# Kernel optimization log

Hardware: AMD Instinct MI355X
Metric: run time of the kernel (lower is better)

## Reference

```python
import jax, jax.numpy as jnp
import numpy as np

B, L, T, H, NH, NQ = 4096, 64, 48, 64, 4, 3
HD = H // NH  # head dim = 16


def lstm_layer(x, h0, c0, Wih, Whh, bih, bhh):
    # x: (B, S, I); h0, c0: (B, H). PyTorch gate order: i, f, g, o.
    def step(carry, xt):
        h, c = carry
        g = xt @ Wih.T + bih + h @ Whh.T + bhh
        i, f, gg, o = jnp.split(g, 4, axis=-1)
        c = jax.nn.sigmoid(f) * c + jax.nn.sigmoid(i) * jnp.tanh(gg)
        h = jax.nn.sigmoid(o) * jnp.tanh(c)
        return (h, c), h
    (hT, cT), hs = jax.lax.scan(step, (h0, c0), jnp.swapaxes(x, 0, 1))
    return jnp.swapaxes(hs, 0, 1), hT, cT


def lstm2(x, params, h0, c0):
    # params: list of 2 tuples (Wih, Whh, bih, bhh); h0, c0: (2, B, H)
    out = x
    hs, cs = [], []
    for l in range(2):
        Wih, Whh, bih, bhh = params[l]
        out, h, c = lstm_layer(out, h0[l], c0[l], Wih, Whh, bih, bhh)
        hs.append(h)
        cs.append(c)
    return out, jnp.stack(hs), jnp.stack(cs)


def mha(q, k, v, Wqkv, bqkv, Wo, bo):
    # PyTorch nn.MultiheadAttention, batch_first, averaged attn weights.
    Wq, Wk, Wv = jnp.split(Wqkv, 3, axis=0)
    bq, bk, bv = jnp.split(bqkv, 3, axis=0)
    def heads(t):
        b, s, _ = t.shape
        return t.reshape(b, s, NH, HD)
    qh = heads(q @ Wq.T + bq)
    kh = heads(k @ Wk.T + bk)
    vh = heads(v @ Wv.T + bv)
    scores = jnp.einsum('bqhd,bkhd->bhqk', qh, kh) / jnp.sqrt(jnp.float32(HD))
    w = jax.nn.softmax(scores, axis=-1)                      # (B, NH, Sq, Sk)
    out = jnp.einsum('bhqk,bkhd->bqhd', w, vh).reshape(q.shape[0], q.shape[1], H)
    return out @ Wo.T + bo, w.mean(axis=1)                   # averaged over heads


def setup_inputs() -> dict:
    key = jax.random.key(0)
    ks = iter(jax.random.split(key, 32))
    s = 0.08
    d = {
        'x': jax.random.normal(next(ks), (B, L, H), jnp.float32),
        'target': jax.random.normal(next(ks), (B, T, H), jnp.float32),
    }
    for pre in ('enc', 'dec'):
        for l in range(2):
            d[f'{pre}_Wih{l}'] = jax.random.normal(next(ks), (4 * H, H), jnp.float32) * s
            d[f'{pre}_Whh{l}'] = jax.random.normal(next(ks), (4 * H, H), jnp.float32) * s
            d[f'{pre}_bih{l}'] = jnp.zeros((4 * H,), jnp.float32)
            d[f'{pre}_bhh{l}'] = jnp.zeros((4 * H,), jnp.float32)
    d['attn_Wqkv'] = jax.random.normal(next(ks), (3 * H, H), jnp.float32) * s
    d['attn_bqkv'] = jnp.zeros((3 * H,), jnp.float32)
    d['attn_Wo'] = jax.random.normal(next(ks), (H, H), jnp.float32) * s
    d['attn_bo'] = jnp.zeros((H,), jnp.float32)
    d['fc_W1'] = jax.random.normal(next(ks), (H // 2, H), jnp.float32) * s
    d['fc_b1'] = jnp.zeros((H // 2,), jnp.float32)
    d['fc_W2'] = jax.random.normal(next(ks), (NQ, H // 2), jnp.float32) * s
    d['fc_b2'] = jnp.zeros((NQ,), jnp.float32)
    return d


def reference(x, target,
              enc_Wih0, enc_Whh0, enc_bih0, enc_bhh0,
              enc_Wih1, enc_Whh1, enc_bih1, enc_bhh1,
              dec_Wih0, dec_Whh0, dec_bih0, dec_bhh0,
              dec_Wih1, dec_Whh1, dec_bih1, dec_bhh1,
              attn_Wqkv, attn_bqkv, attn_Wo, attn_bo,
              fc_W1, fc_b1, fc_W2, fc_b2):
    enc_p = [(enc_Wih0, enc_Whh0, enc_bih0, enc_bhh0),
             (enc_Wih1, enc_Whh1, enc_bih1, enc_bhh1)]
    dec_p = [(dec_Wih0, dec_Whh0, dec_bih0, dec_bhh0),
             (dec_Wih1, dec_Whh1, dec_bih1, dec_bhh1)]
    z = jnp.zeros((2, x.shape[0], H), x.dtype)
    enc_out, h_n, c_n = lstm2(x, enc_p, z, z)               # (B, L, H)
    attn0, _ = mha(enc_out, enc_out, enc_out, attn_Wqkv, attn_bqkv, attn_Wo, attn_bo)
    # teacher forcing: step t>=1 consumes target[:, t-1]; step 0 the attended encoder summary
    dec_in = jnp.concatenate([attn0[:, -1:, :], target[:, :-1, :]], axis=1)  # (B, T, H)
    dec_out, _, _ = lstm2(dec_in, dec_p, h_n, c_n)          # (B, T, H)
    attn_out, attn_w = mha(dec_out, enc_out, enc_out, attn_Wqkv, attn_bqkv, attn_Wo, attn_bo)
    pred = jax.nn.relu(attn_out @ fc_W1.T + fc_b1) @ fc_W2.T + fc_b2  # (B, T, 3)
    return pred, attn_w                                      # (B,T,3), (B,T,L)
```

## Files before the change

kernel.cpp:

```cpp
#include <hip/hip_runtime.h>
#include <hip/hip_bf16.h>
#include <cstddef>


#define B_   4096
#define L_   64
#define T_   48
#define H_   64
#define ROWS 16
#define PADH 136

using half8  = __attribute__((ext_vector_type(8))) _Float16;
using half4  = __attribute__((ext_vector_type(4))) _Float16;
using f32x4  = __attribute__((ext_vector_type(4))) float;

#define IC_ 4.8828125e-4f

__device__ __forceinline__ float fsig(float x) {
    return __builtin_amdgcn_rcpf(1.0f + __expf(-x));
}
__device__ __forceinline__ float ftanh(float x) {
    float e = __expf(-2.0f * fabsf(x));
    float r = (1.0f - e) * __builtin_amdgcn_rcpf(1.0f + e);
    return copysignf(r, x);
}

__global__ void transpose_w_all_kernel(
    const float* __restrict__ W0i, const float* __restrict__ W0h,
    const float* __restrict__ W1i, const float* __restrict__ W1h,
    const float* __restrict__ W2i, const float* __restrict__ W2h,
    const float* __restrict__ W3i, const float* __restrict__ W3h,
    _Float16* __restrict__ out) {
    int idx = blockIdx.x * 256 + threadIdx.x;
    int layer = idx >> 14, i = idx & 16383;
    const float* Wi = (layer == 0) ? W0i : (layer == 1) ? W1i : (layer == 2) ? W2i : W3i;
    const float* Wh = (layer == 0) ? W0h : (layer == 1) ? W1h : (layer == 2) ? W2h : W3h;
    int r = i >> 6, k = i & 63;
    _Float16* o = out + (size_t)layer * 32768;
    o[r * 128 + k]      = (_Float16)Wi[i];
    o[r * 128 + 64 + k] = (_Float16)Wh[i];
}

__global__ void split_aux_kernel(const float* __restrict__ Wqkv,
                                 const float* __restrict__ Wo,
                                 const float* __restrict__ W1,
                                 _Float16* __restrict__ wqkvh,
                                 _Float16* __restrict__ woh,
                                 _Float16* __restrict__ w1h) {
    int idx = blockIdx.x * 256 + threadIdx.x;
    if (idx < 12288) {
        float v = Wqkv[idx]; _Float16 h = (_Float16)v;
        wqkvh[idx] = h; wqkvh[12288 + idx] = (_Float16)((v - (float)h) * 2048.f);
    } else if (idx < 16384) {
        int i = idx - 12288;
        float v = Wo[i]; _Float16 h = (_Float16)v;
        woh[i] = h; woh[4096 + i] = (_Float16)((v - (float)h) * 2048.f);
    } else if (idx < 18432) {
        int i = idx - 16384;
        float v = W1[i]; _Float16 h = (_Float16)v;
        w1h[i] = h; w1h[2048 + i] = (_Float16)((v - (float)h) * 2048.f);
    }
}

__global__ __launch_bounds__(512, 2) void lstm2_mfma_kernel(
    const float* __restrict__ inseq,
    const float* __restrict__ in0,
    const _Float16* __restrict__ w1half,
    const float* __restrict__ b1ihp, const float* __restrict__ b1hhp,
    const _Float16* __restrict__ w2half,
    const float* __restrict__ b2ihp, const float* __restrict__ b2hhp,
    const float* __restrict__ h01, const float* __restrict__ c01,
    const float* __restrict__ h02, const float* __restrict__ c02,
    float* __restrict__ outseq2,
    _Float16* __restrict__ outh2,
    float* __restrict__ hf1, float* __restrict__ cf1,
    float* __restrict__ hf2, float* __restrict__ cf2,
    int S, int mode)
{
    __shared__ __align__(16) _Float16 A1[2][16 * PADH];
    __shared__ __align__(16) _Float16 A2[2][16 * PADH];

    const int tid  = threadIdx.x;
    const int w    = tid >> 6;
    const int lrow = tid & 15;
    const int lkg  = (tid >> 4) & 3;
    const int row0 = blockIdx.x * ROWS;

    const bool isL2w = (w >= 4);
    const int  wl    = w & 3;
    const int  hcol  = wl * 16 + lrow;

    const _Float16* wsrc = isL2w ? w2half : w1half;
    const float* bihp = isL2w ? b2ihp : b1ihp;
    const float* bhhp = isL2w ? b2hhp : b1hhp;

    half8 whi[4][4];
    #pragma unroll
    for (int kt = 0; kt < 4; ++kt)
        #pragma unroll
        for (int g = 0; g < 4; ++g) {
            const int col = g * 64 + hcol;
            whi[kt][g] = *(const half8*)&wsrc[(size_t)col * 128 + kt * 32 + lkg * 8];
        }
    float bsv[4];
    #pragma unroll
    for (int g = 0; g < 4; ++g)
        bsv[g] = bihp[g * 64 + hcol] + bhhp[g * 64 + hcol];

    float c[4], hlast[4] = {0.f, 0.f, 0.f, 0.f};

    if (!isL2w) {
        #pragma unroll
        for (int q = 0; q < 4; ++q) {
            const int r = 4 * lkg + q;
            const float* p0 = (mode == 1) ? (in0 + (size_t)(row0 + r) * 64)
                                          : (inseq + (size_t)(row0 + r) * S * 64);
            A1[0][r * PADH + hcol] = (_Float16)p0[hcol];
            float hv = h01 ? h01[(size_t)(row0 + r) * 64 + hcol] : 0.f;
            A1[0][r * PADH + 64 + hcol] = (_Float16)hv;
            c[q] = c01 ? c01[(size_t)(row0 + r) * 64 + hcol] : 0.f;
        }
    } else {
        #pragma unroll
        for (int q = 0; q < 4; ++q) {
            const int r = 4 * lkg + q;
            float hv = h02 ? h02[(size_t)(row0 + r) * 64 + hcol] : 0.f;
            A2[0][r * PADH + 64 + hcol] = (_Float16)hv;
            c[q] = c02 ? c02[(size_t)(row0 + r) * 64 + hcol] : 0.f;
        }
    }

    const int aoff = lrow * PADH + lkg * 8;

    for (int i = 0; i <= S; ++i) {
        asm volatile("s_waitcnt lgkmcnt(0)" ::: "memory");
        __builtin_amdgcn_s_barrier();
        __builtin_amdgcn_sched_barrier(0);

        if (!isL2w) {
            if (i < S) {
                float xn[4];
                if (i + 1 < S) {
                    #pragma unroll
                    for (int q = 0; q < 4; ++q) {
                        const int r = 4 * lkg + q;
                        const float* pn = (mode == 1)
                            ? (inseq + ((size_t)(row0 + r) * S + i) * 64)
                            : (inseq + ((size_t)(row0 + r) * S + (i + 1)) * 64);
                        xn[q] = pn[hcol];
                    }
                }
                const _Float16* As = A1[i & 1];
                f32x4 a0[4];
                #pragma unroll
                for (int g = 0; g < 4; ++g)
                    a0[g] = (f32x4){bsv[g], bsv[g], bsv[g], bsv[g]};
                #pragma unroll
                for (int kt = 0; kt < 4; ++kt) {
                    half8 ah = *(const half8*)&As[aoff + kt * 32];
                    #pragma unroll
                    for (int g = 0; g < 4; ++g)
                        a0[g] = __builtin_amdgcn_mfma_f32_16x16x32_f16(ah, whi[kt][g], a0[g], 0, 0, 0);
                }
                _Float16* Ad1 = A1[(i + 1) & 1];
                _Float16* Ad2 = A2[i & 1];
                #pragma unroll
                for (int q = 0; q < 4; ++q) {
                    const int r = 4 * lkg + q;
                    float gi = a0[0][q], gf = a0[1][q], gg = a0[2][q], go = a0[3][q];
                    c[q] = fsig(gf) * c[q] + fsig(gi) * ftanh(gg);
                    float hv = fsig(go) * ftanh(c[q]);
                    hlast[q] = hv;
                    _Float16 hh = (_Float16)hv;
                    Ad1[r * PADH + 64 + hcol] = hh;
                    Ad2[r * PADH + hcol] = hh;
                }
                if (i + 1 < S) {
                    #pragma unroll
                    for (int q = 0; q < 4; ++q) {
                        const int r = 4 * lkg + q;
                        Ad1[r * PADH + hcol] = (_Float16)xn[q];
                    }
                }
            }
        } else {
            const int j = i - 1;
            if (j >= 0 && j < S) {
                const _Float16* As = A2[j & 1];
                f32x4 a0[4];
                #pragma unroll
                for (int g = 0; g < 4; ++g)
                    a0[g] = (f32x4){bsv[g], bsv[g], bsv[g], bsv[g]};
                #pragma unroll
                for (int kt = 0; kt < 4; ++kt) {
                    half8 ah = *(const half8*)&As[aoff + kt * 32];
                    #pragma unroll
                    for (int g = 0; g < 4; ++g)
                        a0[g] = __builtin_amdgcn_mfma_f32_16x16x32_f16(ah, whi[kt][g], a0[g], 0, 0, 0);
                }
                _Float16* Ad = A2[(j + 1) & 1];
                #pragma unroll
                for (int q = 0; q < 4; ++q) {
                    const int r = 4 * lkg + q;
                    float gi = a0[0][q], gf = a0[1][q], gg = a0[2][q], go = a0[3][q];
                    c[q] = fsig(gf) * c[q] + fsig(gi) * ftanh(gg);
                    float hv = fsig(go) * ftanh(c[q]);
                    hlast[q] = hv;
                    _Float16 hh = (_Float16)hv;
                    Ad[r * PADH + 64 + hcol] = hh;
                    const size_t oidx = ((size_t)(row0 + r) * S + j) * 64 + hcol;
                    if (outseq2) outseq2[oidx] = hv;
                    outh2[oidx] = hh;
                }
            }
        }
    }
    if (hf1) {
        float* hdst = isL2w ? hf2 : hf1;
        float* cdst = isL2w ? cf2 : cf1;
        #pragma unroll
        for (int q = 0; q < 4; ++q) {
            const int r = 4 * lkg + q;
            hdst[(size_t)(row0 + r) * 64 + hcol] = hlast[q];
            cdst[(size_t)(row0 + r) * 64 + hcol] = c[q];
        }
    }
}

__device__ __forceinline__ void stage_split(const float* __restrict__ src,
                                            _Float16* dst, int plane,
                                            int row, int c0) {
    #pragma unroll
    for (int u = 0; u < 4; ++u) {
        float4 v = *(const float4*)(src + u * 4);
        half4 hi, lo;
        hi[0] = (_Float16)v.x; lo[0] = (_Float16)((v.x - (float)hi[0]) * 2048.f);
        hi[1] = (_Float16)v.y; lo[1] = (_Float16)((v.y - (float)hi[1]) * 2048.f);
        hi[2] = (_Float16)v.z; lo[2] = (_Float16)((v.z - (float)hi[2]) * 2048.f);
        hi[3] = (_Float16)v.w; lo[3] = (_Float16)((v.w - (float)hi[3]) * 2048.f);
        *(half4*)&dst[row * 72 + c0 + u * 4] = hi;
        *(half4*)&dst[plane + row * 72 + c0 + u * 4] = lo;
    }
}

__global__ __launch_bounds__(256) void attn0_mfma(
    const float* __restrict__ encout,
    const _Float16* __restrict__ wqkvh,
    const float* __restrict__ bqkv,
    const float* __restrict__ Wqkv,
    const float* __restrict__ Wo,
    const float* __restrict__ bo,
    float* __restrict__ a0last)
{
    __shared__ __align__(16) _Float16 E16[2 * 4608];
    __shared__ __align__(16) _Float16 K16[2 * 4608];
    __shared__ __align__(16) _Float16 V16[4608];
    __shared__ float qv[64];
    __shared__ float wrow[4 * 68];
    __shared__ float ov[64];

    const int b = blockIdx.x, tid = threadIdx.x;
    const int w = tid >> 6, l = tid & 63, lr = l & 15, lkg = l >> 4;

    {
        int row = tid >> 2, c0 = (tid & 3) * 16;
        stage_split(encout + (size_t)b * 4096 + row * 64 + c0, E16, 4608, row, c0);
    }
    __syncthreads();

    for (int tt = w; tt < 8; tt += 4) {
        const int kind = (tt < 4) ? 0 : 1;
        const int mrow = (kind ? tt - 4 : tt) * 16;
        const int wrowB = kind ? 128 : 64;
        half8 ah[2], al[2];
        #pragma unroll
        for (int kt = 0; kt < 2; ++kt) {
            int ao = (mrow + lr) * 72 + kt * 32 + lkg * 8;
            ah[kt] = *(const half8*)&E16[ao];
            al[kt] = *(const half8*)&E16[4608 + ao];
        }
        #pragma unroll
        for (int nt = 0; nt < 4; ++nt) {
            const int col = nt * 16 + lr;
            const float bv = bqkv[wrowB + col];
            f32x4 a0 = (f32x4){bv, bv, bv, bv};
            f32x4 a1 = (f32x4){0.f, 0.f, 0.f, 0.f};
            #pragma unroll
            for (int kt = 0; kt < 2; ++kt) {
                const _Float16* wp = wqkvh + (size_t)(wrowB + col) * 64 + kt * 32 + lkg * 8;
                half8 bh = *(const half8*)wp;
                half8 bl = *(const half8*)(wp + 12288);
                a0 = __builtin_amdgcn_mfma_f32_16x16x32_f16(ah[kt], bh, a0, 0, 0, 0);
                a1 = __builtin_amdgcn_mfma_f32_16x16x32_f16(ah[kt], bl, a1, 0, 0, 0);
                a1 = __builtin_amdgcn_mfma_f32_16x16x32_f16(al[kt], bh, a1, 0, 0, 0);
            }
            #pragma unroll
            for (int i = 0; i < 4; ++i) {
                float g = a0[i] + a1[i] * IC_;
                int r = mrow + lkg * 4 + i;
                if (kind == 0) {
                    _Float16 gh = (_Float16)g;
                    K16[r * 72 + col] = gh;
                    K16[4608 + r * 72 + col] = (_Float16)((g - (float)gh) * 2048.f);
                } else {
                    V16[r * 72 + col] = (_Float16)g;
                }
            }
        }
    }
    if (w == 3) {
        float a = bqkv[l];
        for (int k = 0; k < 64; ++k) {
            float e = (float)E16[63 * 72 + k] + (float)E16[4608 + 63 * 72 + k] * IC_;
            a += e * Wqkv[l * 64 + k];
        }
        qv[l] = a;
    }
    __syncthreads();

    {
        const int h = tid >> 6, kv = tid & 63;
        float s = 0.f;
        #pragma unroll
        for (int d = 0; d < 16; ++d) {
            float kk = (float)K16[kv * 72 + h * 16 + d]
                     + (float)K16[4608 + kv * 72 + h * 16 + d] * IC_;
            s += qv[h * 16 + d] * kk;
        }
        s *= 0.25f;
        float m = s;
        #pragma unroll
        for (int off = 32; off; off >>= 1) m = fmaxf(m, __shfl_xor(m, off));
        float e = __expf(s - m);
        float sum = e;
        #pragma unroll
        for (int off = 32; off; off >>= 1) sum += __shfl_xor(sum, off);
        wrow[h * 68 + kv] = e / sum;
    }
    __syncthreads();
    if (tid < 64) {
        const int h = tid >> 4, d = tid & 15;
        float o = 0.f;
        for (int kv = 0; kv < 64; ++kv)
            o += wrow[h * 68 + kv] * (float)V16[kv * 72 + h * 16 + d];
        ov[tid] = o;
    }
    __syncthreads();
    if (tid < 64) {
        float a = bo[tid];
        for (int k = 0; k < 64; ++k) a += ov[k] * Wo[tid * 64 + k];
        a0last[(size_t)b * 64 + tid] = a;
    }
}

__global__ __launch_bounds__(256, 4) void cross_attn_v3(
    const _Float16* __restrict__ ench, const _Float16* __restrict__ dech,
    const _Float16* __restrict__ wqkvh, const float* __restrict__ bqkv,
    const _Float16* __restrict__ woh,   const float* __restrict__ bo,
    const _Float16* __restrict__ w1h,   const float* __restrict__ b1,
    const float* __restrict__ W2,       const float* __restrict__ b2,
    float* __restrict__ pred, float* __restrict__ attnw)
{
    extern __shared__ __align__(16) char smem[];
    _Float16* E  = (_Float16*)(smem);
    _Float16* D  = (_Float16*)(smem + 9216);
    _Float16* K  = (_Float16*)(smem + 16128);
    _Float16* Q  = (_Float16*)(smem + 25344);
    _Float16* VT = (_Float16*)(smem + 32256);
    _Float16* AO = (_Float16*)(smem + 32256);
    float*    Hl = (float*)(smem + 32256);

    const int b = blockIdx.x, tid = threadIdx.x;
    const int w = tid >> 6, l = tid & 63, lr = l & 15, lkg = l >> 4;
    const int h = w;

    {
        int row = tid >> 2, c0 = (tid & 3) * 16;
        const _Float16* ep = ench + (size_t)b * 4096 + row * 64 + c0;
        *(half8*)&E[row * 72 + c0]     = *(const half8*)ep;
        *(half8*)&E[row * 72 + c0 + 8] = *(const half8*)(ep + 8);
        if (row < 48) {
            const _Float16* dp = dech + (size_t)b * 3072 + row * 64 + c0;
            *(half8*)&D[row * 72 + c0]     = *(const half8*)dp;
            *(half8*)&D[row * 72 + c0 + 8] = *(const half8*)(dp + 8);
        }
    }
    __syncthreads();

    for (int tt = w; tt < 11; tt += 4) {
        const int kind = (tt < 4) ? 0 : ((tt < 8) ? 1 : 2);
        const int mrow = ((kind == 0) ? tt : (kind == 1) ? tt - 4 : tt - 8) * 16;
        const int wrowB = (kind == 0) ? 64 : ((kind == 1) ? 128 : 0);
        const _Float16* S = (kind == 2) ? D : E;
        half8 ah[2];
        #pragma unroll
        for (int kt = 0; kt < 2; ++kt)
            ah[kt] = *(const half8*)&S[(mrow + lr) * 72 + kt * 32 + lkg * 8];
        #pragma unroll
        for (int nt = 0; nt < 4; ++nt) {
            const int col = nt * 16 + lr;
            const float bv = bqkv[wrowB + col];
            f32x4 a0 = (f32x4){bv, bv, bv, bv};
            #pragma unroll
            for (int kt = 0; kt < 2; ++kt) {
                half8 bh = *(const half8*)&wqkvh[(size_t)(wrowB + col) * 64 + kt * 32 + lkg * 8];
                a0 = __builtin_amdgcn_mfma_f32_16x16x32_f16(ah[kt], bh, a0, 0, 0, 0);
            }
            if (kind == 1) {
                half4 p;
                #pragma unroll
                for (int i = 0; i < 4; ++i) p[i] = (_Float16)a0[i];
                *(half4*)&VT[col * 68 + mrow + lkg * 4] = p;
            } else {
                _Float16* dst = (kind == 0) ? K : Q;
                #pragma unroll
                for (int i = 0; i < 4; ++i)
                    dst[(mrow + lkg * 4 + i) * 72 + col] = (_Float16)a0[i];
            }
        }
    }
    __syncthreads();

    const half8 z = {0, 0, 0, 0, 0, 0, 0, 0};
    half8 ka[4], qb[3];
    #pragma unroll
    for (int kvt = 0; kvt < 4; ++kvt)
        ka[kvt] = (lkg < 2) ? *(const half8*)&K[(kvt * 16 + lr) * 72 + h * 16 + lkg * 8] : z;
    #pragma unroll
    for (int qt = 0; qt < 3; ++qt)
        qb[qt] = (lkg < 2) ? *(const half8*)&Q[(qt * 16 + lr) * 72 + h * 16 + lkg * 8] : z;
    __syncthreads();

    _Float16* strip = (_Float16*)(smem + ((h == 0) ? 0 : (h == 1) ? 9216
                                        : (h == 2) ? 16128 : 25344));
    {
        f32x4 s[3][4];
        #pragma unroll
        for (int qt = 0; qt < 3; ++qt) {
            #pragma unroll
            for (int kvt = 0; kvt < 4; ++kvt) {
                f32x4 a0 = (f32x4){0.f, 0.f, 0.f, 0.f};
                a0 = __builtin_amdgcn_mfma_f32_16x16x32_f16(ka[kvt], qb[qt], a0, 0, 0, 0);
                s[qt][kvt] = a0 * 0.25f;
            }
            float m = s[qt][0][0];
            #pragma unroll
            for (int kvt = 0; kvt < 4; ++kvt)
                #pragma unroll
                for (int i = 0; i < 4; ++i) m = fmaxf(m, s[qt][kvt][i]);
            m = fmaxf(m, __shfl_xor(m, 16));
            m = fmaxf(m, __shfl_xor(m, 32));
            float sum = 0.f;
            #pragma unroll
            for (int kvt = 0; kvt < 4; ++kvt)
                #pragma unroll
                for (int i = 0; i < 4; ++i) {
                    float e = __expf(s[qt][kvt][i] - m);
                    s[qt][kvt][i] = e;
                    sum += e;
                }
            sum += __shfl_xor(sum, 16);
            sum += __shfl_xor(sum, 32);
            const float r = 1.0f / sum;
            #pragma unroll
            for (int kvt = 0; kvt < 4; ++kvt) {
                half4 p;
                #pragma unroll
                for (int i = 0; i < 4; ++i) p[i] = (_Float16)(s[qt][kvt][i] * r);
                *(half4*)&strip[(qt * 16 + lr) * 72 + kvt * 16 + lkg * 4] = p;
            }
        }
    }
    f32x4 pv[3];
    {
        half8 vb[2];
        #pragma unroll
        for (int kt = 0; kt < 2; ++kt) {
            half4 lo4 = *(const half4*)&VT[(h * 16 + lr) * 68 + kt * 32 + lkg * 8];
            half4 hi4 = *(const half4*)&VT[(h * 16 + lr) * 68 + kt * 32 + lkg * 8 + 4];
            #pragma unroll
            for (int j = 0; j < 4; ++j) { vb[kt][j] = lo4[j]; vb[kt][4 + j] = hi4[j]; }
        }
        #pragma unroll
        for (int qt = 0; qt < 3; ++qt) {
            f32x4 acc = (f32x4){0.f, 0.f, 0.f, 0.f};
            #pragma unroll
            for (int kt = 0; kt < 2; ++kt) {
                half8 wa = *(const half8*)&strip[(qt * 16 + lr) * 72 + kt * 32 + lkg * 8];
                acc = __builtin_amdgcn_mfma_f32_16x16x32_f16(wa, vb[kt], acc, 0, 0, 0);
            }
            pv[qt] = acc;
        }
    }
    __syncthreads();

    #pragma unroll
    for (int qt = 0; qt < 3; ++qt)
        #pragma unroll
        for (int i = 0; i < 4; ++i)
            AO[(qt * 16 + lkg * 4 + i) * 72 + h * 16 + lr] = (_Float16)pv[qt][i];
    __syncthreads();

    if (w < 3) {
        half8 bAO[2];
        #pragma unroll
        for (int kt = 0; kt < 2; ++kt)
            bAO[kt] = *(const half8*)&AO[(w * 16 + lr) * 72 + kt * 32 + lkg * 8];
        f32x4 ov[4];
        #pragma unroll
        for (int nt = 0; nt < 4; ++nt) {
            f32x4 acc = *(const f32x4*)&bo[nt * 16 + lkg * 4];
            #pragma unroll
            for (int kt = 0; kt < 2; ++kt) {
                half8 aW = *(const half8*)&woh[(size_t)(nt * 16 + lr) * 64 + kt * 32 + lkg * 8];
                acc = __builtin_amdgcn_mfma_f32_16x16x32_f16(aW, bAO[kt], acc, 0, 0, 0);
            }
            ov[nt] = acc;
        }
        #pragma unroll
        for (int nt = 0; nt < 4; ++nt) {
            half4 p;
            #pragma unroll
            for (int i = 0; i < 4; ++i) p[i] = (_Float16)ov[nt][i];
            *(half4*)&AO[(w * 16 + lr) * 72 + nt * 16 + lkg * 4] = p;
        }
        half8 bO[2];
        #pragma unroll
        for (int kt = 0; kt < 2; ++kt)
            bO[kt] = *(const half8*)&AO[(w * 16 + lr) * 72 + kt * 32 + lkg * 8];
        #pragma unroll
        for (int nt = 0; nt < 2; ++nt) {
            f32x4 acc = *(const f32x4*)&b1[nt * 16 + lkg * 4];
            #pragma unroll
            for (int kt = 0; kt < 2; ++kt) {
                half8 aW = *(const half8*)&w1h[(size_t)(nt * 16 + lr) * 64 + kt * 32 + lkg * 8];
                acc = __builtin_amdgcn_mfma_f32_16x16x32_f16(aW, bO[kt], acc, 0, 0, 0);
            }
            f32x4 rl;
            #pragma unroll
            for (int i = 0; i < 4; ++i) rl[i] = fmaxf(acc[i], 0.f);
            *(f32x4*)&Hl[(w * 16 + lr) * 36 + nt * 16 + lkg * 4] = rl;
        }
        if (l < 48) {
            const int qr = l / 3, n = l - 3 * qr;
            const int q = w * 16 + qr;
            float a = b2[n];
            #pragma unroll
            for (int m2 = 0; m2 < 32; ++m2) a += Hl[q * 36 + m2] * W2[n * 32 + m2];
            pred[((size_t)b * 48 + q) * 3 + n] = a;
        }
    } else {
        const _Float16* s0 = (const _Float16*)(smem);
        const _Float16* s1 = (const _Float16*)(smem + 9216);
        const _Float16* s2 = (const _Float16*)(smem + 16128);
        const _Float16* s3 = (const _Float16*)(smem + 25344);
        #pragma unroll 4
        for (int it = 0; it < 48; ++it) {
            int idx = l + it * 64;
            int o = (idx >> 6) * 72 + (idx & 63);
            attnw[(size_t)b * 3072 + idx] =
                0.25f * ((float)s0[o] + (float)s1[o] + (float)s2[o] + (float)s3[o]);
        }
    }
}

extern "C" void kernel_launch(void* const* d_in, const int* in_sizes, int n_in,
                              void* d_out, int out_size, void* d_ws, size_t ws_size,
                              hipStream_t stream) {
    const float* x      = (const float*)d_in[0];
    const float* target = (const float*)d_in[1];
    const float* eWih0 = (const float*)d_in[2],  *eWhh0 = (const float*)d_in[3];
    const float* ebih0 = (const float*)d_in[4],  *ebhh0 = (const float*)d_in[5];
    const float* eWih1 = (const float*)d_in[6],  *eWhh1 = (const float*)d_in[7];
    const float* ebih1 = (const float*)d_in[8],  *ebhh1 = (const float*)d_in[9];
    const float* dWih0 = (const float*)d_in[10], *dWhh0 = (const float*)d_in[11];
    const float* dbih0 = (const float*)d_in[12], *dbhh0 = (const float*)d_in[13];
    const float* dWih1 = (const float*)d_in[14], *dWhh1 = (const float*)d_in[15];
    const float* dbih1 = (const float*)d_in[16], *dbhh1 = (const float*)d_in[17];
    const float* Wqkv = (const float*)d_in[18], *bqkv = (const float*)d_in[19];
    const float* Wo   = (const float*)d_in[20], *bo   = (const float*)d_in[21];
    const float* W1   = (const float*)d_in[22], *b1   = (const float*)d_in[23];
    const float* W2   = (const float*)d_in[24], *b2   = (const float*)d_in[25];

    float* ws = (float*)d_ws;
    float* hseq1  = ws;
    float* encout = hseq1  + (size_t)B_ * L_ * H_;
    float* decout = encout + (size_t)B_ * L_ * H_;
    float* a0last = decout + (size_t)B_ * T_ * H_;
    float* hfin   = a0last + (size_t)B_ * H_;
    float* cfin   = hfin   + (size_t)2 * B_ * H_;
    float* wtg    = cfin   + (size_t)2 * B_ * H_;
    float* auxw   = wtg    + (size_t)4 * 32768;

    _Float16* wh0 = (_Float16*)(wtg);
    _Float16* wh1 = wh0 + 32768;
    _Float16* wh2 = wh1 + 32768;
    _Float16* wh3 = wh2 + 32768;
    _Float16* wqkvh = (_Float16*)auxw;
    _Float16* woh   = wqkvh + 24576;
    _Float16* w1h   = woh + 8192;
    _Float16* encouth = (_Float16*)hseq1;
    _Float16* decouth = encouth + (size_t)B_ * L_ * H_;

    float* pred  = (float*)d_out;
    float* attnw = pred + (size_t)B_ * T_ * 3;

    transpose_w_all_kernel<<<256, 256, 0, stream>>>(
        eWih0, eWhh0, eWih1, eWhh1, dWih0, dWhh0, dWih1, dWhh1, wh0);
    split_aux_kernel<<<72, 256, 0, stream>>>(Wqkv, Wo, W1, wqkvh, woh, w1h);

    lstm2_mfma_kernel<<<B_ / ROWS, 512, 0, stream>>>(
        x, nullptr, wh0, ebih0, ebhh0, wh1, ebih1, ebhh1,
        nullptr, nullptr, nullptr, nullptr,
        encout, encouth, hfin, cfin, hfin + (size_t)B_ * H_, cfin + (size_t)B_ * H_,
        L_, 0);
    attn0_mfma<<<B_, 256, 0, stream>>>(encout, wqkvh, bqkv, Wqkv, Wo, bo, a0last);
    lstm2_mfma_kernel<<<B_ / ROWS, 512, 0, stream>>>(
        target, a0last, wh2, dbih0, dbhh0, wh3, dbih1, dbhh1,
        hfin, cfin, hfin + (size_t)B_ * H_, cfin + (size_t)B_ * H_,
        nullptr, decouth, nullptr, nullptr, nullptr, nullptr, T_, 1);
    cross_attn_v3<<<B_, 256, 40960, stream>>>(
        encouth, decouth, wqkvh, bqkv, woh, bo, w1h, b1, W2, b2, pred, attnw);
}
```

Baseline: 318.5 us.

## Rewrite first-step attention to read fp16 encoder output and parallelize tail

New measurement: 278.7 us. 1.14x faster.

```diff
diff --git a/kernel.cpp b/kernel.cpp
--- a/kernel.cpp
+++ b/kernel.cpp
@@ -46,7 +46,8 @@
                                  const float* __restrict__ W1,
                                  _Float16* __restrict__ wqkvh,
                                  _Float16* __restrict__ woh,
-                                 _Float16* __restrict__ w1h) {
+                                 _Float16* __restrict__ w1h,
+                                 float* __restrict__ woT) {
     int idx = blockIdx.x * 256 + threadIdx.x;
     if (idx < 12288) {
         float v = Wqkv[idx]; _Float16 h = (_Float16)v;
@@ -59,6 +60,9 @@
         int i = idx - 16384;
         float v = W1[i]; _Float16 h = (_Float16)v;
         w1h[i] = h; w1h[2048 + i] = (_Float16)((v - (float)h) * 2048.f);
+    } else if (idx < 22528) {
+        int i = idx - 18432; int r = i >> 6, k = i & 63;
+        woT[k * 64 + r] = Wo[i];
     }
 }
 
@@ -227,106 +231,65 @@
     }
 }
 
-__device__ __forceinline__ void stage_split(const float* __restrict__ src,
-                                            _Float16* dst, int plane,
-                                            int row, int c0) {
-    #pragma unroll
-    for (int u = 0; u < 4; ++u) {
-        float4 v = *(const float4*)(src + u * 4);
-        half4 hi, lo;
-        hi[0] = (_Float16)v.x; lo[0] = (_Float16)((v.x - (float)hi[0]) * 2048.f);
-        hi[1] = (_Float16)v.y; lo[1] = (_Float16)((v.y - (float)hi[1]) * 2048.f);
-        hi[2] = (_Float16)v.z; lo[2] = (_Float16)((v.z - (float)hi[2]) * 2048.f);
-        hi[3] = (_Float16)v.w; lo[3] = (_Float16)((v.w - (float)hi[3]) * 2048.f);
-        *(half4*)&dst[row * 72 + c0 + u * 4] = hi;
-        *(half4*)&dst[plane + row * 72 + c0 + u * 4] = lo;
-    }
-}
-
-__global__ __launch_bounds__(256) void attn0_mfma(
-    const float* __restrict__ encout,
+__global__ __launch_bounds__(256, 4) void attn0_v2(
+    const _Float16* __restrict__ ench,
     const _Float16* __restrict__ wqkvh,
     const float* __restrict__ bqkv,
-    const float* __restrict__ Wqkv,
-    const float* __restrict__ Wo,
+    const float* __restrict__ woT,
     const float* __restrict__ bo,
     float* __restrict__ a0last)
 {
-    __shared__ __align__(16) _Float16 E16[2 * 4608];
-    __shared__ __align__(16) _Float16 K16[2 * 4608];
-    __shared__ __align__(16) _Float16 V16[4608];
-    __shared__ float qv[64];
-    __shared__ float wrow[4 * 68];
+    __shared__ __align__(16) _Float16 E[64 * 72];
+    __shared__ __align__(16) _Float16 K[64 * 72];
+    __shared__ __align__(16) _Float16 V[64 * 72];
+    __shared__ __align__(16) _Float16 Q[64 * 72];
+    __shared__ float wsm[4 * 68];
     __shared__ float ov[64];
+    __shared__ float part[4 * 64];
 
     const int b = blockIdx.x, tid = threadIdx.x;
     const int w = tid >> 6, l = tid & 63, lr = l & 15, lkg = l >> 4;
 
     {
         int row = tid >> 2, c0 = (tid & 3) * 16;
-        stage_split(encout + (size_t)b * 4096 + row * 64 + c0, E16, 4608, row, c0);
-    }
-    __syncthreads();
-
-    for (int tt = w; tt < 8; tt += 4) {
-        const int kind = (tt < 4) ? 0 : 1;
-        const int mrow = (kind ? tt - 4 : tt) * 16;
-        const int wrowB = kind ? 128 : 64;
-        half8 ah[2], al[2];
-        #pragma unroll
-        for (int kt = 0; kt < 2; ++kt) {
-            int ao = (mrow + lr) * 72 + kt * 32 + lkg * 8;
-            ah[kt] = *(const half8*)&E16[ao];
-            al[kt] = *(const half8*)&E16[4608 + ao];
-        }
+        const _Float16* ep = ench + (size_t)b * 4096 + row * 64 + c0;
+        *(half8*)&E[row * 72 + c0]     = *(const half8*)ep;
+        *(half8*)&E[row * 72 + c0 + 8] = *(const half8*)(ep + 8);
+    }
+    __syncthreads();
+
+    for (int tt = w; tt < 12; tt += 4) {
+        const int kind = tt >> 2;
+        const int mrow = (tt & 3) * 16;
+        const int wrowB = (kind == 0) ? 64 : ((kind == 1) ? 128 : 0);
+        half8 ah[2];
+        #pragma unroll
+        for (int kt = 0; kt < 2; ++kt)
+            ah[kt] = *(const half8*)&E[(mrow + lr) * 72 + kt * 32 + lkg * 8];
+        _Float16* dst = (kind == 0) ? K : ((kind == 1) ? V : Q);
         #pragma unroll
         for (int nt = 0; nt < 4; ++nt) {
             const int col = nt * 16 + lr;
             const float bv = bqkv[wrowB + col];
             f32x4 a0 = (f32x4){bv, bv, bv, bv};
-            f32x4 a1 = (f32x4){0.f, 0.f, 0.f, 0.f};
             #pragma unroll
             for (int kt = 0; kt < 2; ++kt) {
-                const _Float16* wp = wqkvh + (size_t)(wrowB + col) * 64 + kt * 32 + lkg * 8;
-                half8 bh = *(const half8*)wp;
-                half8 bl = *(const half8*)(wp + 12288);
+                half8 bh = *(const half8*)&wqkvh[(size_t)(wrowB + col) * 64 + kt * 32 + lkg * 8];
                 a0 = __builtin_amdgcn_mfma_f32_16x16x32_f16(ah[kt], bh, a0, 0, 0, 0);
-                a1 = __builtin_amdgcn_mfma_f32_16x16x32_f16(ah[kt], bl, a1, 0, 0, 0);
-                a1 = __builtin_amdgcn_mfma_f32_16x16x32_f16(al[kt], bh, a1, 0, 0, 0);
-            }
-            #pragma unroll
-            for (int i = 0; i < 4; ++i) {
-                float g = a0[i] + a1[i] * IC_;
-                int r = mrow + lkg * 4 + i;
-                if (kind == 0) {
-                    _Float16 gh = (_Float16)g;
-                    K16[r * 72 + col] = gh;
-                    K16[4608 + r * 72 + col] = (_Float16)((g - (float)gh) * 2048.f);
-                } else {
-                    V16[r * 72 + col] = (_Float16)g;
-                }
-            }
-        }
-    }
-    if (w == 3) {
-        float a = bqkv[l];
-        for (int k = 0; k < 64; ++k) {
-            float e = (float)E16[63 * 72 + k] + (float)E16[4608 + 63 * 72 + k] * IC_;
-            a += e * Wqkv[l * 64 + k];
-        }
-        qv[l] = a;
+            }
+            #pragma unroll
+            for (int i = 0; i < 4; ++i)
+                dst[(mrow + lkg * 4 + i) * 72 + col] = (_Float16)a0[i];
+        }
     }
     __syncthreads();
 
     {
-        const int h = tid >> 6, kv = tid & 63;
+        const int kv = l;
         float s = 0.f;
         #pragma unroll
-        for (int d = 0; d < 16; ++d) {
-            float kk = (float)K16[kv * 72 + h * 16 + d]
-                     + (float)K16[4608 + kv * 72 + h * 16 + d] * IC_;
-            s += qv[h * 16 + d] * kk;
-        }
+        for (int d = 0; d < 16; ++d)
+            s += (float)Q[63 * 72 + w * 16 + d] * (float)K[kv * 72 + w * 16 + d];
         s *= 0.25f;
         float m = s;
         #pragma unroll
@@ -335,20 +298,37 @@
         float sum = e;
         #pragma unroll
         for (int off = 32; off; off >>= 1) sum += __shfl_xor(sum, off);
-        wrow[h * 68 + kv] = e / sum;
+        wsm[w * 68 + kv] = e / sum;
+    }
+    __syncthreads();
+
+    {
+        const int d = l & 15, gr = l >> 4;
+        float o = 0.f;
+        #pragma unroll
+        for (int k = 0; k < 16; ++k) {
+            const int kv = gr * 16 + k;
+            o += wsm[w * 68 + kv] * (float)V[kv * 72 + w * 16 + d];
+        }
+        o += __shfl_xor(o, 16);
+        o += __shfl_xor(o, 32);
+        if (l < 16) ov[w * 16 + l] = o;
+    }
+    __syncthreads();
+
+    {
+        const int j = tid & 63, g = tid >> 6;
+        float p = 0.f;
+        #pragma unroll
+        for (int k = 0; k < 16; ++k) {
+            const int kk = g * 16 + k;
+            p += ov[kk] * woT[kk * 64 + j];
+        }
+        part[g * 64 + j] = p;
     }
     __syncthreads();
     if (tid < 64) {
-        const int h = tid >> 4, d = tid & 15;
-        float o = 0.f;
-        for (int kv = 0; kv < 64; ++kv)
-            o += wrow[h * 68 + kv] * (float)V16[kv * 72 + h * 16 + d];
-        ov[tid] = o;
-    }
-    __syncthreads();
-    if (tid < 64) {
-        float a = bo[tid];
-        for (int k = 0; k < 64; ++k) a += ov[k] * Wo[tid * 64 + k];
+        float a = bo[tid] + part[tid] + part[64 + tid] + part[128 + tid] + part[192 + tid];
         a0last[(size_t)b * 64 + tid] = a;
     }
 }
@@ -599,6 +579,7 @@
     _Float16* wqkvh = (_Float16*)auxw;
     _Float16* woh   = wqkvh + 24576;
     _Float16* w1h   = woh + 8192;
+    float*    woT   = auxw + 18432;
     _Float16* encouth = (_Float16*)hseq1;
     _Float16* decouth = encouth + (size_t)B_ * L_ * H_;
 
@@ -607,14 +588,14 @@
 
     transpose_w_all_kernel<<<256, 256, 0, stream>>>(
         eWih0, eWhh0, eWih1, eWhh1, dWih0, dWhh0, dWih1, dWhh1, wh0);
-    split_aux_kernel<<<72, 256, 0, stream>>>(Wqkv, Wo, W1, wqkvh, woh, w1h);
+    split_aux_kernel<<<88, 256, 0, stream>>>(Wqkv, Wo, W1, wqkvh, woh, w1h, woT);
 
     lstm2_mfma_kernel<<<B_ / ROWS, 512, 0, stream>>>(
         x, nullptr, wh0, ebih0, ebhh0, wh1, ebih1, ebhh1,
         nullptr, nullptr, nullptr, nullptr,
-        encout, encouth, hfin, cfin, hfin + (size_t)B_ * H_, cfin + (size_t)B_ * H_,
+        nullptr, encouth, hfin, cfin, hfin + (size_t)B_ * H_, cfin + (size_t)B_ * H_,
         L_, 0);
-    attn0_mfma<<<B_, 256, 0, stream>>>(encout, wqkvh, bqkv, Wqkv, Wo, bo, a0last);
+    attn0_v2<<<B_, 256, 0, stream>>>(encouth, wqkvh, bqkv, woT, bo, a0last);
     lstm2_mfma_kernel<<<B_ / ROWS, 512, 0, stream>>>(
         target, a0last, wh2, dbih0, dbhh0, wh3, dbih1, dbhh1,
         hfin, cfin, hfin + (size_t)B_ * H_, cfin + (size_t)B_ * H_,
```
